# Performance work log

Measured on AMD Instinct MI355X. Metric: run time of the kernel, lower is better.

The kernel has to match this reference:

```python
import jax, jax.numpy as jnp
import numpy as np

N_USERS = 100000
N_ITEMS = 40000
N_NODES = N_USERS + N_ITEMS
EMB = 128
BATCH = 8192
N_EDGES = 1000000  # user-item interactions; symmetric graph has 2*N_EDGES nnz
N_LAYERS = 3
ALPHA = 0.1
GAMMA = 0.01


def _make_graph(edge_user, edge_item):
    # symmetric bipartite adjacency in COO: rows/cols over [0, N_NODES)
    rows = jnp.concatenate([edge_user, edge_item + N_USERS])
    cols = jnp.concatenate([edge_item + N_USERS, edge_user])
    return rows, cols


def setup_inputs() -> dict:
    key = jax.random.key(0)
    ks = jax.random.split(key, 8)
    user_emb = jax.random.normal(ks[0], (N_USERS, EMB), dtype=jnp.float32) * 0.1
    item_emb = jax.random.normal(ks[1], (N_ITEMS, EMB), dtype=jnp.float32) * 0.1
    edge_user = jax.random.randint(ks[2], (N_EDGES,), 0, N_USERS)
    edge_item = jax.random.randint(ks[3], (N_EDGES,), 0, N_ITEMS)
    # D^{-1/2} A D^{-1/2} normalization values (LightGCN getSparseGraph)
    rows, cols = _make_graph(edge_user, edge_item)
    deg = jax.ops.segment_sum(jnp.ones_like(rows, dtype=jnp.float32), rows,
                              num_segments=N_NODES)
    inv_sqrt = jnp.where(deg > 0, 1.0 / jnp.sqrt(jnp.maximum(deg, 1.0)), 0.0)
    graph_vals = inv_sqrt[rows] * inv_sqrt[cols]  # [2*N_EDGES]
    users = jax.random.randint(ks[4], (BATCH,), 0, N_USERS)
    pos_items = jax.random.randint(ks[5], (BATCH,), 0, N_ITEMS)
    neg_items = jax.random.randint(ks[6], (BATCH,), 0, N_ITEMS)
    k7, k8 = jax.random.split(ks[7])
    sampled_user = jax.random.randint(k7, (2 * BATCH,), 0, N_USERS)
    sampled_items = jax.random.randint(k8, (2 * BATCH,), 0, N_ITEMS)
    return {"user_emb": user_emb, "item_emb": item_emb, "graph_vals": graph_vals,
            "edge_user": edge_user, "edge_item": edge_item, "users": users,
            "pos_items": pos_items, "neg_items": neg_items,
            "sampled_user": sampled_user, "sampled_items": sampled_items}


def _lightgcn_compute(user_emb, item_emb, rows, cols, vals):
    all_emb = jnp.concatenate([user_emb, item_emb], axis=0)  # [N_NODES, EMB]
    acc = all_emb
    for _ in range(N_LAYERS):
        # SpMM: out[r] += v * x[c]
        all_emb = jax.ops.segment_sum(vals[:, None] * all_emb[cols], rows,
                                      num_segments=N_NODES)
        acc = acc + all_emb
    light_out = acc / jnp.float32(N_LAYERS + 1)  # mean over stacked layers
    return light_out[:N_USERS], light_out[N_USERS:]


def reference(user_emb, item_emb, graph_vals, edge_user, edge_item,
              users, pos_items, neg_items, sampled_user, sampled_items):
    rows, cols = _make_graph(edge_user, edge_item)
    all_users, all_items = _lightgcn_compute(user_emb, item_emb, rows, cols, graph_vals)

    u = all_users[users]                       # [B, D]
    pos = all_items[pos_items]                 # [B, D]
    neg = all_items[neg_items]                 # [B, D]
    all_e = jnp.concatenate([pos, neg], axis=0)            # [2B, D]
    u2 = jnp.concatenate([u, u], axis=0)                   # [2B, D]
    pred = jax.nn.sigmoid(jnp.sum(u2 * all_e, axis=1))     # [2B]
    labels = jnp.concatenate([jnp.ones((pos.shape[0],), jnp.float32),
                              jnp.zeros((neg.shape[0],), jnp.float32)])
    eps = 0.0
    bce_loss = -jnp.mean(labels * jnp.log(pred) + (1.0 - labels) * jnp.log(1.0 - pred))

    su = all_users[sampled_user]
    si = all_items[sampled_items]
    pred_ul = jax.nn.sigmoid(jnp.sum(su * si, axis=1))
    logp_hat = jnp.log(pred)
    pred_avg = jnp.mean(pred)
    pred_ul_avg = jnp.mean(pred_ul)
    info_loss = ALPHA * (-pred_avg * jnp.log(pred_ul_avg)
                         - (1.0 - pred_avg) * jnp.log(1.0 - pred_ul_avg)) \
                + GAMMA * jnp.mean(pred * logp_hat)
    return bce_loss, info_loss
```

## Files before the change

### kernel.cpp

```cpp
#include <hip/hip_runtime.h>
#include <math.h>

#define N_USERS 100000
#define N_ITEMS 40000
#define N_NODES (N_USERS + N_ITEMS)
#define EMB 128
#define EMBQ (EMB / 4)
#define EMBH (EMB / 2)
#define BATCH 8192
#define N_EDGES 1000000
#define ALPHA 0.1f
#define GAMMA 0.01f
#define FP8_SCALE 32.0f
#define INV_FP8_SCALE (1.0f / FP8_SCALE)

#define RB_U 512
#define NB_U ((N_USERS + RB_U - 1) / RB_U)
#define RB_I 256
#define NB_I ((N_ITEMS + RB_I - 1) / RB_I)
#define NB_T (NB_U + NB_I)
#define PART_BLOCKS 256

#define CSRU_MAX (N_EDGES + 4 * (NB_U * RB_U))
#define CSRI_MAX (N_EDGES + 4 * (NB_I * RB_I))

#define UBLK8 ((N_USERS + 7) / 8)
#define IBLK8 ((N_ITEMS + 7) / 8)

typedef float f32x2 __attribute__((ext_vector_type(2)));

__device__ inline unsigned int f2bf(float x) {
    const unsigned int b = __float_as_uint(x);
    return (b + 0x7FFFu + ((b >> 16) & 1u)) >> 16;
}
__device__ inline float bfl(unsigned int w) { return __uint_as_float(w << 16); }
__device__ inline float bfh(unsigned int w) { return __uint_as_float(w & 0xFFFF0000u); }

__device__ inline void acc4(unsigned int v, float& s0, float& s1, float& s2, float& s3) {
    const f32x2 lo = __builtin_amdgcn_cvt_pk_f32_fp8((int)v, false);
    const f32x2 hi = __builtin_amdgcn_cvt_pk_f32_fp8((int)v, true);
    s0 += lo.x; s1 += lo.y; s2 += hi.x; s3 += hi.y;
}


__global__ void bucketA(const int* __restrict__ eu, const int* __restrict__ ev,
                        int* __restrict__ histA ) {
    __shared__ int h[NB_T];
    for (int k = threadIdx.x; k < NB_T; k += 256) h[k] = 0;
    __syncthreads();
    const int b = blockIdx.x;
    const int beg = (int)((long long)N_EDGES * b / PART_BLOCKS);
    const int end = (int)((long long)N_EDGES * (b + 1) / PART_BLOCKS);
    for (int i = beg + threadIdx.x; i < end; i += 256) {
        const int u = __builtin_nontemporal_load(&eu[i]);
        const int v = __builtin_nontemporal_load(&ev[i]);
        atomicAdd(&h[u >> 9], 1);
        atomicAdd(&h[NB_U + (v >> 8)], 1);
    }
    __syncthreads();
    for (int k = threadIdx.x; k < NB_T; k += 256) histA[b * NB_T + k] = h[k];
}

__global__ void bucketB1(const int* __restrict__ histA, int* __restrict__ woff,
                         int* __restrict__ bktCnt) {
    const int k = blockIdx.x;
    const int t = threadIdx.x;
    const int lane = t & 63, wid = t >> 6;
    const int v = histA[t * NB_T + k];
    int x = v;
    #pragma unroll
    for (int off = 1; off < 64; off <<= 1) {
        const int y = __shfl_up(x, off);
        if (lane >= off) x += y;
    }
    __shared__ int wt[4];
    if (lane == 63) wt[wid] = x;
    __syncthreads();
    int wo = 0;
    for (int q = 0; q < wid; ++q) wo += wt[q];
    woff[t * NB_T + k] = wo + x - v;
    if (t == 255) bktCnt[k] = wo + x;
}

__global__ void scan353(const int* __restrict__ in, int* __restrict__ base_out,
                        int* __restrict__ tot_u, int* __restrict__ tot_i) {
    const int t = threadIdx.x;
    const int lane = t & 63, wid = t >> 6;
    const int v = (t < NB_T) ? in[t] : 0;
    int x = v;
    #pragma unroll
    for (int off = 1; off < 64; off <<= 1) {
        const int y = __shfl_up(x, off);
        if (lane >= off) x += y;
    }
    __shared__ int wt[8];
    if (lane == 63) wt[wid] = x;
    __syncthreads();
    int wo = 0;
    for (int q = 0; q < wid; ++q) wo += wt[q];
    const int inc = wo + x;
    __shared__ int uTot, aTot;
    if (t == NB_U - 1) uTot = inc;
    if (t == NB_T - 1) aTot = inc;
    __syncthreads();
    if (t < NB_U)      base_out[t] = inc - v;
    else if (t < NB_T) base_out[t] = inc - v - uTot;
    if (t == 0) {
        if (tot_u) *tot_u = uTot;
        if (tot_i) *tot_i = aTot - uTot;
    }
}

__global__ void bucketC(const int* __restrict__ eu, const int* __restrict__ ev,
                        const int* __restrict__ woff,
                        const int* __restrict__ bktBase,
                        unsigned int* __restrict__ part_u,
                        unsigned int* __restrict__ part_i) {
    __shared__ int cur[NB_T];
    const int b = blockIdx.x;
    for (int k = threadIdx.x; k < NB_T; k += 256)
        cur[k] = woff[b * NB_T + k] + bktBase[k];
    __syncthreads();
    const int beg = (int)((long long)N_EDGES * b / PART_BLOCKS);
    const int end = (int)((long long)N_EDGES * (b + 1) / PART_BLOCKS);
    for (int i = beg + threadIdx.x; i < end; i += 256) {
        const int u = __builtin_nontemporal_load(&eu[i]);
        const int v = __builtin_nontemporal_load(&ev[i]);
        const int pu = atomicAdd(&cur[u >> 9], 1);
        part_u[pu] = (unsigned int)((u & (RB_U - 1)) | (v << 9));
        const int pi = atomicAdd(&cur[NB_U + (v >> 8)], 1);
        part_i[pi] = (unsigned int)((v & (RB_I - 1)) | (u << 8));
    }
}

__global__ void csr_d1(const unsigned int* __restrict__ part_u,
                       const unsigned int* __restrict__ part_i,
                       const int* __restrict__ bktBase, const int* __restrict__ bktCnt,
                       int* __restrict__ deg, float* __restrict__ isq_u,
                       float* __restrict__ isq_i,
                       int* __restrict__ rs_u, int* __restrict__ rs_i,
                       int* __restrict__ bps) {
    const int k = blockIdx.x;
    const bool isU = (k < NB_U);
    const int R = isU ? RB_U : RB_I;
    const int row0 = isU ? k * RB_U : (k - NB_U) * RB_I;
    const int Nside = isU ? N_USERS : N_ITEMS;
    const unsigned int* part = isU ? part_u : part_i;
    const int mask = R - 1;
    __shared__ int dh[RB_U];
    for (int r = threadIdx.x; r < R; r += 256) dh[r] = 0;
    __syncthreads();
    const int base = bktBase[k], cnt = bktCnt[k];
    for (int j = threadIdx.x; j < cnt; j += 256)
        atomicAdd(&dh[part[base + j] & mask], 1);
    __syncthreads();
    const int t = threadIdx.x, lane = t & 63, wid = t >> 6;
    const int r0 = 2 * t, r1 = 2 * t + 1;
    const int d0 = (r0 < R) ? dh[r0] : 0;
    const int d1 = (r1 < R) ? dh[r1] : 0;
    const int v0 = (d0 + 3) & ~3, v1 = (d1 + 3) & ~3;
    const int s = v0 + v1;
    int x = s;
    #pragma unroll
    for (int off = 1; off < 64; off <<= 1) {
        const int y = __shfl_up(x, off);
        if (lane >= off) x += y;
    }
    __shared__ int wtot[4];
    if (lane == 63) wtot[wid] = x;
    __syncthreads();
    int wo = 0;
    for (int q = 0; q < wid; ++q) wo += wtot[q];
    const int pref = wo + x - s;
    if (t == 0) bps[k] = wtot[0] + wtot[1] + wtot[2] + wtot[3];
    if (r0 < R && row0 + r0 < Nside) {
        deg[(isU ? 0 : N_USERS) + row0 + r0] = d0;
        if (isU) { isq_u[row0 + r0] = (d0 > 0) ? (1.0f / sqrtf((float)d0)) : 0.f;
                   rs_u[row0 + r0] = pref; }
        else     { isq_i[row0 + r0] = (d0 > 0) ? (1.0f / sqrtf((float)d0)) : 0.f;
                   rs_i[row0 + r0] = pref; }
    }
    if (r1 < R && row0 + r1 < Nside) {
        deg[(isU ? 0 : N_USERS) + row0 + r1] = d1;
        if (isU) { isq_u[row0 + r1] = (d1 > 0) ? (1.0f / sqrtf((float)d1)) : 0.f;
                   rs_u[row0 + r1] = pref + v0; }
        else     { isq_i[row0 + r1] = (d1 > 0) ? (1.0f / sqrtf((float)d1)) : 0.f;
                   rs_i[row0 + r1] = pref + v0; }
    }
}

__global__ void csr_scatter(const unsigned int* __restrict__ part_u,
                            const unsigned int* __restrict__ part_i,
                            const int* __restrict__ bktBase, const int* __restrict__ bktCnt,
                            const int* __restrict__ bcb,
                            int* __restrict__ rs_u, int* __restrict__ rs_i,
                            const int* __restrict__ deg,
                            unsigned short* __restrict__ csr_u, int* __restrict__ csr_i) {
    const int k = blockIdx.x;
    const bool isU = (k < NB_U);
    const int R = isU ? RB_U : RB_I;
    const int row0 = isU ? k * RB_U : (k - NB_U) * RB_I;
    const int Nside = isU ? N_USERS : N_ITEMS;
    const unsigned int* part = isU ? part_u : part_i;
    int* rs = isU ? rs_u : rs_i;
    const int* dg = isU ? deg : deg + N_USERS;
    const int mask = R - 1;
    const int shift = isU ? 9 : 8;
    __shared__ int cur[RB_U];
    const int cb = bcb[k];
    for (int r = threadIdx.x; r < R; r += 256) {
        const int row = row0 + r;
        if (row < Nside) {
            const int st = cb + rs[row];
            rs[row] = st;
            cur[r] = st;
            const int d = dg[row];
            const int dp = (d + 3) & ~3;
            for (int q = d; q < dp; ++q) {
                if (isU) csr_u[st + q] = (unsigned short)N_ITEMS;
                else     csr_i[st + q] = N_USERS;
            }
        } else cur[r] = 0;
    }
    __syncthreads();
    const int base = bktBase[k], cnt = bktCnt[k];
    for (int j = threadIdx.x; j < cnt; j += 256) {
        const unsigned int e = part[base + j];
        const int pos = atomicAdd(&cur[e & mask], 1);
        const int col = (int)(e >> shift);
        if (isU) csr_u[pos] = (unsigned short)col; else csr_i[pos] = col;
    }
}


__global__ void init_kernel(const float* __restrict__ user_emb,
                            const float* __restrict__ item_emb,
                            const float* __restrict__ isq_u,
                            const float* __restrict__ isq_i,
                            unsigned int* __restrict__ e0u,
                            unsigned int* __restrict__ e0i,
                            unsigned int* __restrict__ e1u,
                            unsigned int* __restrict__ e2u,
                            unsigned int* __restrict__ e3u,
                            unsigned int* __restrict__ e1i,
                            unsigned int* __restrict__ e2i,
                            unsigned int* __restrict__ e3i,
                            unsigned int* __restrict__ x0b) {
    if (blockIdx.x == 0 && threadIdx.x < 256) {
        const int t = threadIdx.x;
        unsigned int* bufs[8] = {e0u, e1u, e2u, e3u, e0i, e1i, e2i, e3i};
        const int b = t >> 5;
        const size_t row = (b < 4) ? (size_t)N_USERS : (size_t)N_ITEMS;
        bufs[b][row * EMBQ + (t & 31)] = 0u;
    }
    const int total = N_NODES * EMBQ;
    const int utotal = N_USERS * EMBQ;
    int i = blockIdx.x * blockDim.x + threadIdx.x;
    const int stride = gridDim.x * blockDim.x;
    for (; i < total; i += stride) {
        const int node = i >> 5;
        const int q    = i & 31;
        float4 v; float n;
        if (node < N_USERS) {
            v = ((const float4*)(user_emb + (size_t)node * EMB))[q];
            n = FP8_SCALE * isq_u[node];
        } else {
            v = ((const float4*)(item_emb + (size_t)(node - N_USERS) * EMB))[q];
            n = FP8_SCALE * isq_i[node - N_USERS];
        }
        int pk = __builtin_amdgcn_cvt_pk_fp8_f32(n * v.x, n * v.y, 0, false);
        pk = __builtin_amdgcn_cvt_pk_fp8_f32(n * v.z, n * v.w, pk, true);
        if (node < N_USERS) e0u[i] = (unsigned int)pk;
        else                e0i[i - utotal] = (unsigned int)pk;
        const size_t xb = (size_t)node * EMBH + q * 2;
        x0b[xb]     = f2bf(v.x) | (f2bf(v.y) << 16);
        x0b[xb + 1] = f2bf(v.z) | (f2bf(v.w) << 16);
    }
}

__global__ void spmm_fused(const unsigned int* __restrict__ cur_u,
                           const unsigned int* __restrict__ cur_i,
                           unsigned int* __restrict__ nxt_u,
                           unsigned int* __restrict__ nxt_i,
                           const int* __restrict__ rs_u,
                           const int* __restrict__ rs_i,
                           const unsigned short* __restrict__ csr_u,
                           const int* __restrict__ csr_i,
                           const float* __restrict__ isq_u,
                           const float* __restrict__ isq_i) {
    const int lane = threadIdx.x & 63;
    const int half = lane >> 5;
    const int sub  = lane & 31;
    const int b = blockIdx.x;
    const int hw = (threadIdx.x >> 6) * 2 + half;
    float s0 = 0.f, s1 = 0.f, s2 = 0.f, s3 = 0.f;
    if (b < UBLK8) {
        const int w = b * 8 + hw;
        if (w >= N_USERS) return;
        const int beg = rs_u[w];
        const int end = rs_u[w + 1];
        int j = beg;
        for (; j + 8 <= end; j += 8) {
            const ushort4 ca = *(const ushort4*)(csr_u + j);
            const ushort4 cb = *(const ushort4*)(csr_u + j + 4);
            const unsigned int v0 = cur_i[(size_t)ca.x * EMBQ + sub];
            const unsigned int v1 = cur_i[(size_t)ca.y * EMBQ + sub];
            const unsigned int v2 = cur_i[(size_t)ca.z * EMBQ + sub];
            const unsigned int v3 = cur_i[(size_t)ca.w * EMBQ + sub];
            const unsigned int v4 = cur_i[(size_t)cb.x * EMBQ + sub];
            const unsigned int v5 = cur_i[(size_t)cb.y * EMBQ + sub];
            const unsigned int v6 = cur_i[(size_t)cb.z * EMBQ + sub];
            const unsigned int v7 = cur_i[(size_t)cb.w * EMBQ + sub];
            acc4(v0, s0, s1, s2, s3); acc4(v1, s0, s1, s2, s3);
            acc4(v2, s0, s1, s2, s3); acc4(v3, s0, s1, s2, s3);
            acc4(v4, s0, s1, s2, s3); acc4(v5, s0, s1, s2, s3);
            acc4(v6, s0, s1, s2, s3); acc4(v7, s0, s1, s2, s3);
        }
        if (j < end) {
            const ushort4 cc = *(const ushort4*)(csr_u + j);
            const unsigned int v0 = cur_i[(size_t)cc.x * EMBQ + sub];
            const unsigned int v1 = cur_i[(size_t)cc.y * EMBQ + sub];
            const unsigned int v2 = cur_i[(size_t)cc.z * EMBQ + sub];
            const unsigned int v3 = cur_i[(size_t)cc.w * EMBQ + sub];
            acc4(v0, s0, s1, s2, s3); acc4(v1, s0, s1, s2, s3);
            acc4(v2, s0, s1, s2, s3); acc4(v3, s0, s1, s2, s3);
        }
        const float n = isq_u[w];
        const float sc = n * n;
        int pk = __builtin_amdgcn_cvt_pk_fp8_f32(sc * s0, sc * s1, 0, false);
        pk = __builtin_amdgcn_cvt_pk_fp8_f32(sc * s2, sc * s3, pk, true);
        nxt_u[(size_t)w * EMBQ + sub] = (unsigned int)pk;
    } else {
        const int w = (b - UBLK8) * 8 + hw;
        if (w >= N_ITEMS) return;
        const int beg = rs_i[w];
        const int end = rs_i[w + 1];
        int j = beg;
        for (; j + 8 <= end; j += 8) {
            const int4 ca = *(const int4*)(csr_i + j);
            const int4 cb = *(const int4*)(csr_i + j + 4);
            const unsigned int v0 = cur_u[(size_t)ca.x * EMBQ + sub];
            const unsigned int v1 = cur_u[(size_t)ca.y * EMBQ + sub];
            const unsigned int v2 = cur_u[(size_t)ca.z * EMBQ + sub];
            const unsigned int v3 = cur_u[(size_t)ca.w * EMBQ + sub];
            const unsigned int v4 = cur_u[(size_t)cb.x * EMBQ + sub];
            const unsigned int v5 = cur_u[(size_t)cb.y * EMBQ + sub];
            const unsigned int v6 = cur_u[(size_t)cb.z * EMBQ + sub];
            const unsigned int v7 = cur_u[(size_t)cb.w * EMBQ + sub];
            acc4(v0, s0, s1, s2, s3); acc4(v1, s0, s1, s2, s3);
            acc4(v2, s0, s1, s2, s3); acc4(v3, s0, s1, s2, s3);
            acc4(v4, s0, s1, s2, s3); acc4(v5, s0, s1, s2, s3);
            acc4(v6, s0, s1, s2, s3); acc4(v7, s0, s1, s2, s3);
        }
        if (j < end) {
            const int4 cc = *(const int4*)(csr_i + j);
            const unsigned int v0 = cur_u[(size_t)cc.x * EMBQ + sub];
            const unsigned int v1 = cur_u[(size_t)cc.y * EMBQ + sub];
            const unsigned int v2 = cur_u[(size_t)cc.z * EMBQ + sub];
            const unsigned int v3 = cur_u[(size_t)cc.w * EMBQ + sub];
            acc4(v0, s0, s1, s2, s3); acc4(v1, s0, s1, s2, s3);
            acc4(v2, s0, s1, s2, s3); acc4(v3, s0, s1, s2, s3);
        }
        const float n = isq_i[w];
        const float sc = n * n;
        int pk = __builtin_amdgcn_cvt_pk_fp8_f32(sc * s0, sc * s1, 0, false);
        pk = __builtin_amdgcn_cvt_pk_fp8_f32(sc * s2, sc * s3, pk, true);
        nxt_i[(size_t)w * EMBQ + sub] = (unsigned int)pk;
    }
}

__device__ inline float logsigmoidf(float x) {
    return (x >= 0.f) ? -log1pf(expf(-x)) : (x - log1pf(expf(x)));
}

__global__ void loss_kernel(const unsigned int* __restrict__ x0b,
                            const unsigned short* __restrict__ e1u,
                            const unsigned short* __restrict__ e2u,
                            const unsigned short* __restrict__ e3u,
                            const unsigned short* __restrict__ e1i,
                            const unsigned short* __restrict__ e2i,
                            const unsigned short* __restrict__ e3i,
                            const int* __restrict__ deg,
                            const int* __restrict__ users,
                            const int* __restrict__ pos_items,
                            const int* __restrict__ neg_items,
                            const int* __restrict__ sampled_user,
                            const int* __restrict__ sampled_items,
                            float* __restrict__ sums) {
    const int lane = threadIdx.x & 63;
    const int wid  = threadIdx.x >> 6;
    const int gw   = blockIdx.x * 4 + wid;
    const int nw   = gridDim.x * 4;
    float s_bce = 0.f, s_pred = 0.f, s_plogp = 0.f, s_ul = 0.f;
    for (int p = gw; p < 4 * BATCH; p += nw) {
        int u, it;
        if (p < 2 * BATCH) {
            if (p < BATCH) { u = users[p];          it = pos_items[p]; }
            else           { u = users[p - BATCH];  it = neg_items[p - BATCH]; }
        } else {
            const int q = p - 2 * BATCH;
            u = sampled_user[q]; it = sampled_items[q];
        }
        const float sdu = sqrtf((float)deg[u]) * INV_FP8_SCALE;
        const unsigned int a0 = x0b[(size_t)u * EMBH + lane];
        const size_t ui = (size_t)u * 64 + lane;
        const f32x2 u1 = __builtin_amdgcn_cvt_pk_f32_fp8((int)e1u[ui], false);
        const f32x2 u2 = __builtin_amdgcn_cvt_pk_f32_fp8((int)e2u[ui], false);
        const f32x2 u3 = __builtin_amdgcn_cvt_pk_f32_fp8((int)e3u[ui], false);
        const float ax = bfl(a0) + sdu * (u1.x + u2.x + u3.x);
        const float ay = bfh(a0) + sdu * (u1.y + u2.y + u3.y);
        const float sdi = sqrtf((float)deg[N_USERS + it]) * INV_FP8_SCALE;
        const unsigned int b0 = x0b[(size_t)(N_USERS + it) * EMBH + lane];
        const size_t ii = (size_t)it * 64 + lane;
        const f32x2 i1 = __builtin_amdgcn_cvt_pk_f32_fp8((int)e1i[ii], false);
        const f32x2 i2 = __builtin_amdgcn_cvt_pk_f32_fp8((int)e2i[ii], false);
        const f32x2 i3 = __builtin_amdgcn_cvt_pk_f32_fp8((int)e3i[ii], false);
        const float bx = bfl(b0) + sdi * (i1.x + i2.x + i3.x);
        const float by = bfh(b0) + sdi * (i1.y + i2.y + i3.y);
        float d = ax * bx + ay * by;
        #pragma unroll
        for (int off = 32; off > 0; off >>= 1) d += __shfl_down(d, off);
        if (lane == 0) {
            d *= (1.f / 16.f);
            const float pred = 1.f / (1.f + expf(-d));
            if (p < 2 * BATCH) {
                const float ls  = logsigmoidf(d);
                const float lsn = logsigmoidf(-d);
                s_bce   += (p < BATCH) ? -ls : -lsn;
                s_pred  += pred;
                s_plogp += pred * ls;
            } else {
                s_ul += pred;
            }
        }
    }
    __shared__ float red[4][4];
    if (lane == 0) {
        red[wid][0] = s_bce; red[wid][1] = s_pred;
        red[wid][2] = s_plogp; red[wid][3] = s_ul;
    }
    __syncthreads();
    if (threadIdx.x < 4) {
        const float v = red[0][threadIdx.x] + red[1][threadIdx.x]
                      + red[2][threadIdx.x] + red[3][threadIdx.x];
        atomicAdd(&sums[threadIdx.x], v);
    }
}

__global__ void finalize_kernel(const float* __restrict__ sums, float* __restrict__ out) {
    if (threadIdx.x == 0 && blockIdx.x == 0) {
        const float n = 2.f * BATCH;
        const float bce        = sums[0] / n;
        const float pred_avg   = sums[1] / n;
        const float plogp_avg  = sums[2] / n;
        const float predul_avg = sums[3] / n;
        const float info = ALPHA * (-pred_avg * logf(predul_avg)
                                    - (1.f - pred_avg) * logf(1.f - predul_avg))
                         + GAMMA * plogp_avg;
        out[0] = bce;
        out[1] = info;
    }
}

extern "C" void kernel_launch(void* const* d_in, const int* in_sizes, int n_in,
                              void* d_out, int out_size, void* d_ws, size_t ws_size,
                              hipStream_t stream) {
    const float* user_emb      = (const float*)d_in[0];
    const float* item_emb      = (const float*)d_in[1];
    const int*   edge_user     = (const int*)d_in[3];
    const int*   edge_item     = (const int*)d_in[4];
    const int*   users         = (const int*)d_in[5];
    const int*   pos_items     = (const int*)d_in[6];
    const int*   neg_items     = (const int*)d_in[7];
    const int*   sampled_user  = (const int*)d_in[8];
    const int*   sampled_items = (const int*)d_in[9];
    float* out = (float*)d_out;

    const size_t ebu = (size_t)(N_USERS + 1) * EMBQ * sizeof(unsigned int);
    const size_t ebi = (size_t)(N_ITEMS + 1) * EMBQ * sizeof(unsigned int);
    char* ws = (char*)d_ws;
    size_t off = 0;
    unsigned int* e0u = (unsigned int*)(ws + off); off += ebu;
    unsigned int* e1u = (unsigned int*)(ws + off); off += ebu;
    unsigned int* e2u = (unsigned int*)(ws + off); off += ebu;
    unsigned int* e3u = (unsigned int*)(ws + off); off += ebu;
    unsigned int* e0i = (unsigned int*)(ws + off); off += ebi;
    unsigned int* e1i = (unsigned int*)(ws + off); off += ebi;
    unsigned int* e2i = (unsigned int*)(ws + off); off += ebi;
    unsigned int* e3i = (unsigned int*)(ws + off); off += ebi;
    unsigned int* x0b = (unsigned int*)(ws + off); off += (size_t)N_NODES * EMBH * 4;
    float* sums = (float*)(ws + off); off += 256;
    int*   deg   = (int*)(ws + off); off += (size_t)N_NODES * 4;
    int*   rs_u  = (int*)(ws + off); off += (size_t)(N_USERS + 1) * 4 + 252;
    int*   rs_i  = (int*)(ws + off); off += (size_t)(N_ITEMS + 1) * 4 + 252;
    float* isq_u = (float*)(ws + off); off += (size_t)N_USERS * 4;
    float* isq_i = (float*)(ws + off); off += (size_t)N_ITEMS * 4;
    unsigned short* csr_u = (unsigned short*)(ws + off); off += (size_t)CSRU_MAX * 2 + 256;
    int*   csr_i = (int*)(ws + off); off += (size_t)CSRI_MAX * 4;
    unsigned int* part_u = (unsigned int*)(ws + off); off += (size_t)N_EDGES * 4;
    unsigned int* part_i = (unsigned int*)(ws + off); off += (size_t)N_EDGES * 4;
    int*   histA   = (int*)(ws + off); off += (size_t)PART_BLOCKS * NB_T * 4;
    int*   woff    = (int*)(ws + off); off += (size_t)PART_BLOCKS * NB_T * 4;
    int*   bktCnt  = (int*)(ws + off); off += (size_t)NB_T * 4;
    int*   bktBase = (int*)(ws + off); off += (size_t)NB_T * 4;
    int*   bps     = (int*)(ws + off); off += (size_t)NB_T * 4;
    int*   bcb     = (int*)(ws + off); off += (size_t)NB_T * 4;

    hipMemsetAsync(sums, 0, 4 * sizeof(float), stream);

    bucketA<<<PART_BLOCKS, 256, 0, stream>>>(edge_user, edge_item, histA);
    bucketB1<<<NB_T, 256, 0, stream>>>(histA, woff, bktCnt);
    scan353<<<1, 512, 0, stream>>>(bktCnt, bktBase, nullptr, nullptr);
    bucketC<<<PART_BLOCKS, 256, 0, stream>>>(edge_user, edge_item, woff, bktBase,
                                             part_u, part_i);
    csr_d1<<<NB_T, 256, 0, stream>>>(part_u, part_i, bktBase, bktCnt,
                                     deg, isq_u, isq_i, rs_u, rs_i, bps);
    scan353<<<1, 512, 0, stream>>>(bps, bcb, rs_u + N_USERS, rs_i + N_ITEMS);
    csr_scatter<<<NB_T, 256, 0, stream>>>(part_u, part_i, bktBase, bktCnt, bcb,
                                          rs_u, rs_i, deg, csr_u, csr_i);
    init_kernel<<<4096, 256, 0, stream>>>(user_emb, item_emb, isq_u, isq_i,
                                          e0u, e0i, e1u, e2u, e3u, e1i, e2i, e3i,
                                          x0b);

    spmm_fused<<<UBLK8 + IBLK8, 256, 0, stream>>>(e0u, e0i, e1u, e1i, rs_u, rs_i,
                                                  csr_u, csr_i, isq_u, isq_i);
    spmm_fused<<<UBLK8 + IBLK8, 256, 0, stream>>>(e1u, e1i, e2u, e2i, rs_u, rs_i,
                                                  csr_u, csr_i, isq_u, isq_i);
    spmm_fused<<<UBLK8 + IBLK8, 256, 0, stream>>>(e2u, e2i, e3u, e3i, rs_u, rs_i,
                                                  csr_u, csr_i, isq_u, isq_i);

    loss_kernel<<<512, 256, 0, stream>>>(x0b,
                                         (const unsigned short*)e1u,
                                         (const unsigned short*)e2u,
                                         (const unsigned short*)e3u,
                                         (const unsigned short*)e1i,
                                         (const unsigned short*)e2i,
                                         (const unsigned short*)e3i,
                                         deg, users, pos_items, neg_items,
                                         sampled_user, sampled_items, sums);
    finalize_kernel<<<1, 1, 0, stream>>>(sums, out);
}
```

Baseline: 233.4 us.

## Replace bucket and CSR prefix scans with atomic block-base allocation

The two single-block scan kernels are replaced by atomic ticket counters that hand each bucket and CSR block a base offset in arbitrary order. Because row segments are no longer contiguous in index order, explicit row-end arrays are added and the SpMM reads them. The degree-count and scatter passes are merged into one csr_build kernel, and the memset is folded into bucketA. This cuts several launches and dependent serial steps, at the cost of a nondeterministic CSR layout and one more index array read in SpMM.

```diff
diff --git a/kernel.cpp b/kernel.cpp
--- a/kernel.cpp
+++ b/kernel.cpp
@@ -44,7 +44,12 @@
 
 
 __global__ void bucketA(const int* __restrict__ eu, const int* __restrict__ ev,
-                        int* __restrict__ histA ) {
+                        int* __restrict__ histA ,
+                        float* __restrict__ sums, int* __restrict__ tk) {
+    if (blockIdx.x == 0 && threadIdx.x < 8) {
+        if (threadIdx.x < 4) sums[threadIdx.x] = 0.f;
+        else                 tk[threadIdx.x - 4] = 0;
+    }
     __shared__ int h[NB_T];
     for (int k = threadIdx.x; k < NB_T; k += 256) h[k] = 0;
     __syncthreads();
@@ -62,7 +67,7 @@
 }
 
 __global__ void bucketB1(const int* __restrict__ histA, int* __restrict__ woff,
-                         int* __restrict__ bktCnt) {
+                         int* __restrict__ bktCnt, int* __restrict__ tk) {
     const int k = blockIdx.x;
     const int t = threadIdx.x;
     const int lane = t & 63, wid = t >> 6;
@@ -74,52 +79,33 @@
         if (lane >= off) x += y;
     }
     __shared__ int wt[4];
+    __shared__ int base;
     if (lane == 63) wt[wid] = x;
     __syncthreads();
     int wo = 0;
     for (int q = 0; q < wid; ++q) wo += wt[q];
-    woff[t * NB_T + k] = wo + x - v;
-    if (t == 255) bktCnt[k] = wo + x;
-}
-
-__global__ void scan353(const int* __restrict__ in, int* __restrict__ base_out,
-                        int* __restrict__ tot_u, int* __restrict__ tot_i) {
-    const int t = threadIdx.x;
-    const int lane = t & 63, wid = t >> 6;
-    const int v = (t < NB_T) ? in[t] : 0;
-    int x = v;
-    #pragma unroll
-    for (int off = 1; off < 64; off <<= 1) {
-        const int y = __shfl_up(x, off);
-        if (lane >= off) x += y;
-    }
-    __shared__ int wt[8];
-    if (lane == 63) wt[wid] = x;
-    __syncthreads();
-    int wo = 0;
-    for (int q = 0; q < wid; ++q) wo += wt[q];
-    const int inc = wo + x;
-    __shared__ int uTot, aTot;
-    if (t == NB_U - 1) uTot = inc;
-    if (t == NB_T - 1) aTot = inc;
-    __syncthreads();
-    if (t < NB_U)      base_out[t] = inc - v;
-    else if (t < NB_T) base_out[t] = inc - v - uTot;
-    if (t == 0) {
-        if (tot_u) *tot_u = uTot;
-        if (tot_i) *tot_i = aTot - uTot;
-    }
+    if (t == 255) {
+        const int tot = wo + x;
+        bktCnt[k] = tot;
+        base = atomicAdd(&tk[(k < NB_U) ? 0 : 1], tot);
+    }
+    __syncthreads();
+    woff[t * NB_T + k] = base + wo + x - v;
+}
+
+__global__ void bucketB1b(const int* __restrict__ woff, int* __restrict__ bktBase) {
+    const int k = blockIdx.x * 256 + threadIdx.x;
+    if (k < NB_T) bktBase[k] = woff[k];
 }
 
 __global__ void bucketC(const int* __restrict__ eu, const int* __restrict__ ev,
                         const int* __restrict__ woff,
-                        const int* __restrict__ bktBase,
                         unsigned int* __restrict__ part_u,
                         unsigned int* __restrict__ part_i) {
     __shared__ int cur[NB_T];
     const int b = blockIdx.x;
     for (int k = threadIdx.x; k < NB_T; k += 256)
-        cur[k] = woff[b * NB_T + k] + bktBase[k];
+        cur[k] = woff[b * NB_T + k];
     __syncthreads();
     const int beg = (int)((long long)N_EDGES * b / PART_BLOCKS);
     const int end = (int)((long long)N_EDGES * (b + 1) / PART_BLOCKS);
@@ -133,13 +119,15 @@
     }
 }
 
-__global__ void csr_d1(const unsigned int* __restrict__ part_u,
-                       const unsigned int* __restrict__ part_i,
-                       const int* __restrict__ bktBase, const int* __restrict__ bktCnt,
-                       int* __restrict__ deg, float* __restrict__ isq_u,
-                       float* __restrict__ isq_i,
-                       int* __restrict__ rs_u, int* __restrict__ rs_i,
-                       int* __restrict__ bps) {
+__global__ void csr_build(const unsigned int* __restrict__ part_u,
+                          const unsigned int* __restrict__ part_i,
+                          const int* __restrict__ bktBase, const int* __restrict__ bktCnt,
+                          int* __restrict__ tk,
+                          int* __restrict__ deg, float* __restrict__ isq_u,
+                          float* __restrict__ isq_i,
+                          int* __restrict__ rs_u, int* __restrict__ rs_i,
+                          int* __restrict__ rend_u, int* __restrict__ rend_i,
+                          unsigned short* __restrict__ csr_u, int* __restrict__ csr_i) {
     const int k = blockIdx.x;
     const bool isU = (k < NB_U);
     const int R = isU ? RB_U : RB_I;
@@ -147,7 +135,10 @@
     const int Nside = isU ? N_USERS : N_ITEMS;
     const unsigned int* part = isU ? part_u : part_i;
     const int mask = R - 1;
+    const int shift = isU ? 9 : 8;
     __shared__ int dh[RB_U];
+    __shared__ int cur[RB_U];
+    __shared__ int cbase;
     for (int r = threadIdx.x; r < R; r += 256) dh[r] = 0;
     __syncthreads();
     const int base = bktBase[k], cnt = bktCnt[k];
@@ -172,58 +163,34 @@
     int wo = 0;
     for (int q = 0; q < wid; ++q) wo += wtot[q];
     const int pref = wo + x - s;
-    if (t == 0) bps[k] = wtot[0] + wtot[1] + wtot[2] + wtot[3];
+    if (t == 255) {
+        cbase = atomicAdd(&tk[isU ? 2 : 3], wo + x);
+    }
+    __syncthreads();
+    const int cb = cbase;
     if (r0 < R && row0 + r0 < Nside) {
+        const int st = cb + pref;
         deg[(isU ? 0 : N_USERS) + row0 + r0] = d0;
+        cur[r0] = st;
         if (isU) { isq_u[row0 + r0] = (d0 > 0) ? (1.0f / sqrtf((float)d0)) : 0.f;
-                   rs_u[row0 + r0] = pref; }
+                   rs_u[row0 + r0] = st; rend_u[row0 + r0] = st + v0;
+                   for (int q = d0; q < v0; ++q) csr_u[st + q] = (unsigned short)N_ITEMS; }
         else     { isq_i[row0 + r0] = (d0 > 0) ? (1.0f / sqrtf((float)d0)) : 0.f;
-                   rs_i[row0 + r0] = pref; }
-    }
+                   rs_i[row0 + r0] = st; rend_i[row0 + r0] = st + v0;
+                   for (int q = d0; q < v0; ++q) csr_i[st + q] = N_USERS; }
+    } else if (r0 < R) cur[r0] = 0;
     if (r1 < R && row0 + r1 < Nside) {
+        const int st = cb + pref + v0;
         deg[(isU ? 0 : N_USERS) + row0 + r1] = d1;
+        cur[r1] = st;
         if (isU) { isq_u[row0 + r1] = (d1 > 0) ? (1.0f / sqrtf((float)d1)) : 0.f;
-                   rs_u[row0 + r1] = pref + v0; }
+                   rs_u[row0 + r1] = st; rend_u[row0 + r1] = st + v1;
+                   for (int q = d1; q < v1; ++q) csr_u[st + q] = (unsigned short)N_ITEMS; }
         else     { isq_i[row0 + r1] = (d1 > 0) ? (1.0f / sqrtf((float)d1)) : 0.f;
-                   rs_i[row0 + r1] = pref + v0; }
-    }
-}
-
-__global__ void csr_scatter(const unsigned int* __restrict__ part_u,
-                            const unsigned int* __restrict__ part_i,
-                            const int* __restrict__ bktBase, const int* __restrict__ bktCnt,
-                            const int* __restrict__ bcb,
-                            int* __restrict__ rs_u, int* __restrict__ rs_i,
-                            const int* __restrict__ deg,
-                            unsigned short* __restrict__ csr_u, int* __restrict__ csr_i) {
-    const int k = blockIdx.x;
-    const bool isU = (k < NB_U);
-    const int R = isU ? RB_U : RB_I;
-    const int row0 = isU ? k * RB_U : (k - NB_U) * RB_I;
-    const int Nside = isU ? N_USERS : N_ITEMS;
-    const unsigned int* part = isU ? part_u : part_i;
-    int* rs = isU ? rs_u : rs_i;
-    const int* dg = isU ? deg : deg + N_USERS;
-    const int mask = R - 1;
-    const int shift = isU ? 9 : 8;
-    __shared__ int cur[RB_U];
-    const int cb = bcb[k];
-    for (int r = threadIdx.x; r < R; r += 256) {
-        const int row = row0 + r;
-        if (row < Nside) {
-            const int st = cb + rs[row];
-            rs[row] = st;
-            cur[r] = st;
-            const int d = dg[row];
-            const int dp = (d + 3) & ~3;
-            for (int q = d; q < dp; ++q) {
-                if (isU) csr_u[st + q] = (unsigned short)N_ITEMS;
-                else     csr_i[st + q] = N_USERS;
-            }
-        } else cur[r] = 0;
-    }
-    __syncthreads();
-    const int base = bktBase[k], cnt = bktCnt[k];
+                   rs_i[row0 + r1] = st; rend_i[row0 + r1] = st + v1;
+                   for (int q = d1; q < v1; ++q) csr_i[st + q] = N_USERS; }
+    } else if (r1 < R) cur[r1] = 0;
+    __syncthreads();
     for (int j = threadIdx.x; j < cnt; j += 256) {
         const unsigned int e = part[base + j];
         const int pos = atomicAdd(&cur[e & mask], 1);
@@ -284,6 +251,8 @@
                            unsigned int* __restrict__ nxt_i,
                            const int* __restrict__ rs_u,
                            const int* __restrict__ rs_i,
+                           const int* __restrict__ rend_u,
+                           const int* __restrict__ rend_i,
                            const unsigned short* __restrict__ csr_u,
                            const int* __restrict__ csr_i,
                            const float* __restrict__ isq_u,
@@ -298,7 +267,7 @@
         const int w = b * 8 + hw;
         if (w >= N_USERS) return;
         const int beg = rs_u[w];
-        const int end = rs_u[w + 1];
+        const int end = rend_u[w];
         int j = beg;
         for (; j + 8 <= end; j += 8) {
             const ushort4 ca = *(const ushort4*)(csr_u + j);
@@ -334,7 +303,7 @@
         const int w = (b - UBLK8) * 8 + hw;
         if (w >= N_ITEMS) return;
         const int beg = rs_i[w];
-        const int end = rs_i[w + 1];
+        const int end = rend_i[w];
         int j = beg;
         for (; j + 8 <= end; j += 8) {
             const int4 ca = *(const int4*)(csr_i + j);
@@ -490,9 +459,12 @@
     unsigned int* e3i = (unsigned int*)(ws + off); off += ebi;
     unsigned int* x0b = (unsigned int*)(ws + off); off += (size_t)N_NODES * EMBH * 4;
     float* sums = (float*)(ws + off); off += 256;
+    int*   tk    = (int*)(ws + off); off += 256;
     int*   deg   = (int*)(ws + off); off += (size_t)N_NODES * 4;
-    int*   rs_u  = (int*)(ws + off); off += (size_t)(N_USERS + 1) * 4 + 252;
-    int*   rs_i  = (int*)(ws + off); off += (size_t)(N_ITEMS + 1) * 4 + 252;
+    int*   rs_u  = (int*)(ws + off); off += (size_t)N_USERS * 4;
+    int*   rs_i  = (int*)(ws + off); off += (size_t)N_ITEMS * 4;
+    int*   rend_u = (int*)(ws + off); off += (size_t)N_USERS * 4;
+    int*   rend_i = (int*)(ws + off); off += (size_t)N_ITEMS * 4;
     float* isq_u = (float*)(ws + off); off += (size_t)N_USERS * 4;
     float* isq_i = (float*)(ws + off); off += (size_t)N_ITEMS * 4;
     unsigned short* csr_u = (unsigned short*)(ws + off); off += (size_t)CSRU_MAX * 2 + 256;
@@ -503,31 +475,28 @@
     int*   woff    = (int*)(ws + off); off += (size_t)PART_BLOCKS * NB_T * 4;
     int*   bktCnt  = (int*)(ws + off); off += (size_t)NB_T * 4;
     int*   bktBase = (int*)(ws + off); off += (size_t)NB_T * 4;
-    int*   bps     = (int*)(ws + off); off += (size_t)NB_T * 4;
-    int*   bcb     = (int*)(ws + off); off += (size_t)NB_T * 4;
-
-    hipMemsetAsync(sums, 0, 4 * sizeof(float), stream);
-
-    bucketA<<<PART_BLOCKS, 256, 0, stream>>>(edge_user, edge_item, histA);
-    bucketB1<<<NB_T, 256, 0, stream>>>(histA, woff, bktCnt);
-    scan353<<<1, 512, 0, stream>>>(bktCnt, bktBase, nullptr, nullptr);
-    bucketC<<<PART_BLOCKS, 256, 0, stream>>>(edge_user, edge_item, woff, bktBase,
+
+    bucketA<<<PART_BLOCKS, 256, 0, stream>>>(edge_user, edge_item, histA, sums, tk);
+    bucketB1<<<NB_T, 256, 0, stream>>>(histA, woff, bktCnt, tk);
+    bucketB1b<<<2, 256, 0, stream>>>(woff, bktBase);
+    bucketC<<<PART_BLOCKS, 256, 0, stream>>>(edge_user, edge_item, woff,
                                              part_u, part_i);
-    csr_d1<<<NB_T, 256, 0, stream>>>(part_u, part_i, bktBase, bktCnt,
-                                     deg, isq_u, isq_i, rs_u, rs_i, bps);
-    scan353<<<1, 512, 0, stream>>>(bps, bcb, rs_u + N_USERS, rs_i + N_ITEMS);
-    csr_scatter<<<NB_T, 256, 0, stream>>>(part_u, part_i, bktBase, bktCnt, bcb,
-                                          rs_u, rs_i, deg, csr_u, csr_i);
+    csr_build<<<NB_T, 256, 0, stream>>>(part_u, part_i, bktBase, bktCnt, tk,
+                                        deg, isq_u, isq_i, rs_u, rs_i,
+                                        rend_u, rend_i, csr_u, csr_i);
     init_kernel<<<4096, 256, 0, stream>>>(user_emb, item_emb, isq_u, isq_i,
                                           e0u, e0i, e1u, e2u, e3u, e1i, e2i, e3i,
                                           x0b);
 
     spmm_fused<<<UBLK8 + IBLK8, 256, 0, stream>>>(e0u, e0i, e1u, e1i, rs_u, rs_i,
-                                                  csr_u, csr_i, isq_u, isq_i);
+                                                  rend_u, rend_i, csr_u, csr_i,
+                                                  isq_u, isq_i);
     spmm_fused<<<UBLK8 + IBLK8, 256, 0, stream>>>(e1u, e1i, e2u, e2i, rs_u, rs_i,
-                                                  csr_u, csr_i, isq_u, isq_i);
+                                                  rend_u, rend_i, csr_u, csr_i,
+                                                  isq_u, isq_i);
     spmm_fused<<<UBLK8 + IBLK8, 256, 0, stream>>>(e2u, e2i, e3u, e3i, rs_u, rs_i,
-                                                  csr_u, csr_i, isq_u, isq_i);
+                                                  rend_u, rend_i, csr_u, csr_i,
+                                                  isq_u, isq_i);
 
     loss_kernel<<<512, 256, 0, stream>>>(x0b,
                                          (const unsigned short*)e1u,
```

Measured after the change: 226.7 us. 2.9% less time.
